# Kernel tuning notes

Hardware: AMD Instinct MI355X
Metric: run time of the kernel (lower is better)

The kernel has to match this reference:

```python
import jax, jax.numpy as jnp
import numpy as np

HEADS = 16
DIM_HEAD = 64
LN_EPS = 1e-3  # keras LayerNormalization default


def setup_inputs() -> dict:
    key = jax.random.key(0)
    ks = jax.random.split(key, 4)
    B, N, D = 8, 512, 1024
    inner = HEADS * DIM_HEAD  # 1024
    return {
        "x": jax.random.normal(ks[0], (B, N, D), dtype=jnp.float32),
        "w_qkv": jax.random.normal(ks[1], (D, 3 * inner), dtype=jnp.float32) * (D ** -0.5),
        "reattn_w": jax.random.normal(ks[2], (HEADS, HEADS), dtype=jnp.float32),
        "ln_gamma": jnp.ones((HEADS,), dtype=jnp.float32),
        "ln_beta": jnp.zeros((HEADS,), dtype=jnp.float32),
        "w_out": jax.random.normal(ks[3], (inner, D), dtype=jnp.float32) * (inner ** -0.5),
        "b_out": jnp.zeros((D,), dtype=jnp.float32),
    }


def reference(x, w_qkv, reattn_w, ln_gamma, ln_beta, w_out, b_out):
    B, N, D = x.shape
    H, dh = HEADS, DIM_HEAD
    scale = dh ** -0.5

    qkv = x @ w_qkv  # [B, N, 3*H*dh]
    q, k, v = jnp.split(qkv, 3, axis=-1)
    # b n (h d) -> b h n d
    to_heads = lambda t: t.reshape(B, N, H, dh).transpose(0, 2, 1, 3)
    q, k, v = to_heads(q), to_heads(k), to_heads(v)

    dots = jnp.einsum("bhid,bhjd->bhij", q, k) * scale  # [B, H, N, N]
    attn = jax.nn.softmax(dots, axis=-1)

    # re-attention: mix across heads
    attn = jnp.einsum("bhij,hg->bgij", attn, reattn_w)

    # LayerNorm over the head axis (axis=1), keras default eps
    mean = jnp.mean(attn, axis=1, keepdims=True)
    var = jnp.var(attn, axis=1, keepdims=True)
    attn = (attn - mean) * jax.lax.rsqrt(var + LN_EPS)
    attn = attn * ln_gamma[None, :, None, None] + ln_beta[None, :, None, None]

    out = jnp.einsum("bhij,bhjd->bhid", attn, v)  # [B, H, N, dh]
    out = out.transpose(0, 2, 1, 3).reshape(B, N, H * dh)  # b h n d -> b n (h d)
    return out @ w_out + b_out
```

## Files before the change

### kernel.cpp

```cpp
#include <hip/hip_runtime.h>
#include <math.h>

#define BB 8
#define NN 512
#define DD 1024
#define HH 16
#define DH 64
#define INNER 1024
#define QKV3 3072
#define PSTR (NN * NN + 64)

typedef __attribute__((ext_vector_type(8))) short short8;
typedef __attribute__((ext_vector_type(4))) float f32x4;

#define AS1 __attribute__((address_space(1)))
#define AS3 __attribute__((address_space(3)))

__device__ __forceinline__ float4 ld4(const float* p) { return *(const float4*)p; }

__device__ __forceinline__ unsigned short f2bf(float f) {
    unsigned u = __float_as_uint(f);
    return (unsigned short)((u + 0x7fffu + ((u >> 16) & 1u)) >> 16);
}
__device__ __forceinline__ float bf2f(unsigned short u) {
    return __uint_as_float(((unsigned)u) << 16);
}

__global__ void preprocess(const float* __restrict__ x, unsigned short* __restrict__ xb,
                           const float* __restrict__ wq, unsigned short* __restrict__ wqT,
                           const float* __restrict__ wo, unsigned short* __restrict__ woT) {
    __shared__ float t[32][33];
    const int tid = threadIdx.x;
    const int bx = blockIdx.x;
    if (bx < 4096) {
        size_t i = ((size_t)bx * 256 + tid) * 4;
        float4 v = ld4(x + i);
        ushort4 o;
        o.x = f2bf(v.x); o.y = f2bf(v.y); o.z = f2bf(v.z); o.w = f2bf(v.w);
        *(ushort4*)(xb + i) = o;
        return;
    }
    const float* in; unsigned short* out; int K, N, n0, k0;
    if (bx < 7168) {
        const int bb = bx - 4096;
        in = wq; out = wqT; K = DD; N = QKV3;
        n0 = (bb % 96) * 32; k0 = (bb / 96) * 32;
    } else {
        const int bb = bx - 7168;
        in = wo; out = woT; K = INNER; N = INNER;
        n0 = (bb & 31) * 32; k0 = (bb >> 5) * 32;
    }
    const int tx = tid & 31, ty = tid >> 5;
#pragma unroll
    for (int l = 0; l < 4; ++l)
        t[ty + 8 * l][tx] = in[(size_t)(k0 + ty + 8 * l) * N + n0 + tx];
    __syncthreads();
#pragma unroll
    for (int l = 0; l < 4; ++l)
        out[(size_t)(n0 + ty + 8 * l) * K + k0 + tx] = f2bf(t[tx][ty + 8 * l]);
}

__device__ __forceinline__ void stage128(const unsigned short* __restrict__ A,
                                         const unsigned short* __restrict__ Bt,
                                         int K, int bm, int bn, int kt,
                                         short* sb, int w, int l) {
#pragma unroll
    for (int t = 0; t < 2; ++t) {
        const int q = w * 2 + t;
        const int li = q * 512 + l * 8;
        const int row = li >> 5, kc = li & 31;
        __builtin_amdgcn_global_load_lds(
            (const AS1 void*)(A + (size_t)(bm + row) * K + kt * 32 + kc),
            (AS3 void*)(sb + q * 512), 16, 0, 0);
        __builtin_amdgcn_global_load_lds(
            (const AS1 void*)(Bt + (size_t)(bn + row) * K + kt * 32 + kc),
            (AS3 void*)(sb + 4096 + q * 512), 16, 0, 0);
    }
}

__global__ __launch_bounds__(256) void gemm_bf16(
    const unsigned short* __restrict__ A, const unsigned short* __restrict__ Bt,
    float* __restrict__ C, const float* __restrict__ bias, int M, int N, int K) {
    __shared__ __align__(16) short lds_[2 * 8192];
    const int tid = threadIdx.x;
    const int w = tid >> 6, l = tid & 63;
    const int bm = blockIdx.y * 128, bn = blockIdx.x * 128;
    const int wm = (w >> 1) * 64, wn = (w & 1) * 64;
    const int lrow = l & 15, lq = l >> 4;
    const int NT = K >> 5;

    f32x4 acc[4][4];
#pragma unroll
    for (int i = 0; i < 4; ++i)
#pragma unroll
        for (int j = 0; j < 4; ++j) acc[i][j] = (f32x4){0.f, 0.f, 0.f, 0.f};

    stage128(A, Bt, K, bm, bn, 0, lds_, w, l);
    asm volatile("s_waitcnt vmcnt(0)" ::: "memory");
    __builtin_amdgcn_s_barrier();

    for (int t = 0; t < NT; ++t) {
        const int s = t & 1;
        if (t + 1 < NT)
            stage128(A, Bt, K, bm, bn, t + 1, lds_ + (s ^ 1) * 8192, w, l);
        const short* As_ = lds_ + s * 8192;
        const short* Bs_ = As_ + 4096;
        short8 a[4], b[4];
#pragma unroll
        for (int i = 0; i < 4; ++i)
            a[i] = *(const short8*)(As_ + (wm + i * 16 + lrow) * 32 + lq * 8);
#pragma unroll
        for (int j = 0; j < 4; ++j)
            b[j] = *(const short8*)(Bs_ + (wn + j * 16 + lrow) * 32 + lq * 8);

        asm volatile("s_waitcnt lgkmcnt(0)" ::: "memory");
        __builtin_amdgcn_sched_barrier(0);

        __builtin_amdgcn_s_setprio(1);
#pragma unroll
        for (int i = 0; i < 4; ++i)
#pragma unroll
            for (int j = 0; j < 4; ++j)
                acc[i][j] = __builtin_amdgcn_mfma_f32_16x16x32_bf16(a[i], b[j], acc[i][j], 0, 0, 0);
        __builtin_amdgcn_s_setprio(0);

        asm volatile("s_waitcnt vmcnt(0)" ::: "memory");
        __builtin_amdgcn_s_barrier();
    }

#pragma unroll
    for (int i = 0; i < 4; ++i)
#pragma unroll
        for (int j = 0; j < 4; ++j) {
            const int col = bn + wn + j * 16 + lrow;
            const float bv = bias ? bias[col] : 0.f;
#pragma unroll
            for (int r = 0; r < 4; ++r) {
                const int row = bm + wm + i * 16 + lq * 4 + r;
                C[(size_t)row * N + col] = acc[i][j][r] + bv;
            }
        }
}

__device__ __forceinline__ void stage_st(const unsigned short* __restrict__ G, int K,
                                         int row0, int kt, short* dst_half,
                                         int w, int l) {
    const int grow = row0 + w * 16 + (l >> 2);
    const int gcol = kt * 32 + (((l & 3) * 8) ^ ((l & 32) ? 16 : 0));
    __builtin_amdgcn_global_load_lds(
        (const AS1 void*)(G + (size_t)grow * K + gcol),
        (AS3 void*)(dst_half + w * 512), 16, 0, 0);
}

__global__ __launch_bounds__(512, 2) void gemm256_bf(
    const unsigned short* __restrict__ A, const unsigned short* __restrict__ Bt,
    unsigned short* __restrict__ C, int M, int N, int K) {
    __shared__ __align__(16) short lds_[2 * 16384];
    const int tid = threadIdx.x;
    const int w = tid >> 6, l = tid & 63;
    const int wm = w >> 2, wn = w & 3;
    const int lrow = l & 15, lq = l >> 4;
    const int bm = blockIdx.y * 256, bn = blockIdx.x * 256;
    const int NT = K >> 5;

    const int aoff = lrow * 32 + ((lq * 8) ^ ((lrow & 8) ? 16 : 0));
    const int bsub = (wn & 1) * 4;

    f32x4 acc[8][4];
#pragma unroll
    for (int i = 0; i < 8; ++i)
#pragma unroll
        for (int j = 0; j < 4; ++j) acc[i][j] = (f32x4){0.f, 0.f, 0.f, 0.f};

    stage_st(A,  K, bm,       0, lds_ + 0,     w, l);
    stage_st(A,  K, bm + 128, 0, lds_ + 4096,  w, l);
    stage_st(Bt, K, bn,       0, lds_ + 8192,  w, l);
    stage_st(Bt, K, bn + 128, 0, lds_ + 12288, w, l);
    asm volatile("s_waitcnt vmcnt(0)" ::: "memory");
    __builtin_amdgcn_s_barrier();

    for (int t = 0; t < NT; ++t) {
        const int s = t & 1;
        if (t + 1 < NT) {
            short* nb = lds_ + (s ^ 1) * 16384;
            stage_st(A,  K, bm,       t + 1, nb,         w, l);
            stage_st(A,  K, bm + 128, t + 1, nb + 4096,  w, l);
            stage_st(Bt, K, bn,       t + 1, nb + 8192,  w, l);
            stage_st(Bt, K, bn + 128, t + 1, nb + 12288, w, l);
        }
        const short* Ah = lds_ + s * 16384 + wm * 4096;
        const short* Bh = lds_ + s * 16384 + 8192 + (wn >> 1) * 4096;
        short8 a[8], bfr[4];
#pragma unroll
        for (int i = 0; i < 8; ++i)
            a[i] = *(const short8*)(Ah + i * 512 + aoff);
#pragma unroll
        for (int j = 0; j < 4; ++j)
            bfr[j] = *(const short8*)(Bh + (bsub + j) * 512 + aoff);

        asm volatile("s_waitcnt lgkmcnt(0)" ::: "memory");
        __builtin_amdgcn_sched_barrier(0);

        __builtin_amdgcn_s_setprio(1);
#pragma unroll
        for (int i = 0; i < 8; ++i)
#pragma unroll
            for (int j = 0; j < 4; ++j)
                acc[i][j] = __builtin_amdgcn_mfma_f32_16x16x32_bf16(a[i], bfr[j], acc[i][j], 0, 0, 0);
        __builtin_amdgcn_s_setprio(0);

        asm volatile("s_waitcnt vmcnt(0)" ::: "memory");
        __builtin_amdgcn_s_barrier();
    }

#pragma unroll
    for (int fr = 0; fr < 8; ++fr)
#pragma unroll
        for (int fc = 0; fc < 4; ++fc) {
            const int col = bn + wn * 64 + fc * 16 + lrow;
#pragma unroll
            for (int r = 0; r < 4; ++r) {
                const int row = bm + wm * 128 + fr * 16 + lq * 4 + r;
                C[(size_t)row * N + col] = f2bf(acc[fr][fc][r]);
            }
        }
}

__global__ __launch_bounds__(256) void scores_stream(
    const unsigned short* __restrict__ qkvb, unsigned short* __restrict__ attnb,
    float* __restrict__ lsum2) {
    __shared__ unsigned short Ks[256 * 64];
    __shared__ unsigned short obuf[4][16][68];
    const int bh = blockIdx.x;
    const int h = bh & 15, b = bh >> 4;
    const int jh = blockIdx.y;
    const int w = threadIdx.x >> 6, l = threadIdx.x & 63;
    const int i0 = blockIdx.z * 64 + w * 16;
    const int lrow = l & 15, lq = l >> 4;

    const unsigned short* kbase =
        qkvb + (size_t)(b * NN + jh * 256) * QKV3 + INNER + h * DH;
#pragma unroll
    for (int i = 0; i < 8; ++i) {
        const int r = (w * 8 + i) * 8 + (l >> 3);
        const int c = (l & 7) ^ (r & 7);
        __builtin_amdgcn_global_load_lds(
            (const AS1 void*)(kbase + (size_t)r * QKV3 + c * 8),
            (AS3 void*)(Ks + (w * 8 + i) * 512), 16, 0, 0);
    }

    const unsigned short* qb = qkvb + (size_t)(b * NN) * QKV3 + h * DH + lq * 8;
    const short8 qf0 = *(const short8*)(qb + (size_t)(i0 + lrow) * QKV3);
    const short8 qf1 = *(const short8*)(qb + (size_t)(i0 + lrow) * QKV3 + 32);

    asm volatile("s_waitcnt vmcnt(0)" ::: "memory");
    __syncthreads();

    unsigned short* obase = attnb + (size_t)bh * PSTR + (size_t)i0 * NN + jh * 256;
    const int sw = lrow & 7;
    float lacc = 0.f;
#pragma unroll
    for (int jt = 0; jt < 16; ++jt) {
        const int R = jt * 16 + lrow;
        const short8 kf0 = *(const short8*)(Ks + R * 64 + ((lq ^ sw) * 8));
        const short8 kf1 = *(const short8*)(Ks + R * 64 + (((4 + lq) ^ sw) * 8));
        f32x4 acc = (f32x4){0.f, 0.f, 0.f, 0.f};
        acc = __builtin_amdgcn_mfma_f32_16x16x32_bf16(kf0, qf0, acc, 0, 0, 0);
        acc = __builtin_amdgcn_mfma_f32_16x16x32_bf16(kf1, qf1, acc, 0, 0, 0);
        float e0 = __expf(acc[0] * 0.125f);
        float e1 = __expf(acc[1] * 0.125f);
        float e2 = __expf(acc[2] * 0.125f);
        float e3 = __expf(acc[3] * 0.125f);
        lacc += (e0 + e1) + (e2 + e3);
        ushort4 o;
        o.x = f2bf(e0); o.y = f2bf(e1); o.z = f2bf(e2); o.w = f2bf(e3);
        *(ushort4*)(&obuf[w][lrow][(jt & 3) * 16 + lq * 4]) = o;
        if ((jt & 3) == 3) {
            const int jb = (jt >> 2) * 64;
#pragma unroll
            for (int q = 0; q < 4; ++q) {
                const int rr = q * 4 + (l >> 4);
                const int cc = l & 15;
                *(ushort4*)(obase + (size_t)rr * NN + jb + cc * 4) =
                    *(const ushort4*)(&obuf[w][rr][cc * 4]);
            }
        }
    }
    lacc += __shfl_xor(lacc, 16, 64);
    lacc += __shfl_xor(lacc, 32, 64);
    if (lq == 0)
        lsum2[(size_t)jh * BB * HH * NN + (size_t)bh * NN + i0 + lrow] = lacc;
}

__global__ void reattn_ln_bf(unsigned short* __restrict__ attnb,
                             const float* __restrict__ lsum2,
                             const float* __restrict__ rw,
                             const float* __restrict__ gamma,
                             const float* __restrict__ beta) {
    __shared__ float w[16][16];
    __shared__ float gs[16], bs[16];
    const int tid = threadIdx.x;
    ((float*)w)[tid] = rw[tid];
    if (tid < 16) { gs[tid] = gamma[tid]; bs[tid] = beta[tid]; }
    __syncthreads();

    const size_t idx = (size_t)blockIdx.x * 256 + tid;
    const int j4 = (int)(idx & 127);
    const int i = (int)((idx >> 7) & 511);
    const int b = (int)(idx >> 16);
    unsigned short* base = attnb + (size_t)(b * HH) * PSTR + (size_t)i * NN + j4 * 4;
    const float* l0 = lsum2 + (size_t)(b * HH) * NN + i;
    const float* l1 = l0 + (size_t)BB * HH * NN;

    float v[16][4];
#pragma unroll
    for (int h = 0; h < 16; ++h) {
        const float linv = 1.0f / (l0[h * NN] + l1[h * NN]);
        ushort4 u = *(const ushort4*)(base + (size_t)h * PSTR);
        v[h][0] = bf2f(u.x) * linv; v[h][1] = bf2f(u.y) * linv;
        v[h][2] = bf2f(u.z) * linv; v[h][3] = bf2f(u.w) * linv;
    }
    float o[16][4];
    float me[4] = {0.f, 0.f, 0.f, 0.f};
#pragma unroll
    for (int g = 0; g < 16; ++g) {
        float s0 = 0.f, s1 = 0.f, s2 = 0.f, s3 = 0.f;
#pragma unroll
        for (int h = 0; h < 16; ++h) {
            const float wg = w[h][g];
            s0 += v[h][0] * wg; s1 += v[h][1] * wg;
            s2 += v[h][2] * wg; s3 += v[h][3] * wg;
        }
        o[g][0] = s0; o[g][1] = s1; o[g][2] = s2; o[g][3] = s3;
        me[0] += s0; me[1] += s1; me[2] += s2; me[3] += s3;
    }
#pragma unroll
    for (int r = 0; r < 4; ++r) me[r] *= 0.0625f;
    float va[4] = {0.f, 0.f, 0.f, 0.f};
#pragma unroll
    for (int g = 0; g < 16; ++g)
#pragma unroll
        for (int r = 0; r < 4; ++r) {
            float d = o[g][r] - me[r];
            va[r] += d * d;
        }
    float ri[4];
#pragma unroll
    for (int r = 0; r < 4; ++r) ri[r] = rsqrtf(va[r] * 0.0625f + 1e-3f);
#pragma unroll
    for (int g = 0; g < 16; ++g) {
        ushort4 u;
        u.x = f2bf((o[g][0] - me[0]) * ri[0] * gs[g] + bs[g]);
        u.y = f2bf((o[g][1] - me[1]) * ri[1] * gs[g] + bs[g]);
        u.z = f2bf((o[g][2] - me[2]) * ri[2] * gs[g] + bs[g]);
        u.w = f2bf((o[g][3] - me[3]) * ri[3] * gs[g] + bs[g]);
        *(ushort4*)(base + (size_t)g * PSTR) = u;
    }
}

__global__ void transpose_v(const unsigned short* __restrict__ qkvb,
                            unsigned short* __restrict__ vT) {
    __shared__ unsigned short t[32][33];
    const int bh = blockIdx.z;
    const int h = bh & 15, b = bh >> 4;
    const int j0 = blockIdx.x * 32, d0 = blockIdx.y * 32;
    const int tx = threadIdx.x & 31, ty = threadIdx.x >> 5;
    const unsigned short* src = qkvb + (size_t)(b * NN) * QKV3 + 2 * INNER + h * DH;
#pragma unroll
    for (int k = 0; k < 4; ++k)
        t[ty + 8 * k][tx] = src[(size_t)(j0 + ty + 8 * k) * QKV3 + d0 + tx];
    __syncthreads();
    unsigned short* dst = vT + (size_t)bh * DH * NN;
#pragma unroll
    for (int k = 0; k < 4; ++k)
        dst[(size_t)(d0 + ty + 8 * k) * NN + j0 + tx] = t[tx][ty + 8 * k];
}

__device__ __forceinline__ void stage_pv(const unsigned short* __restrict__ pb,
                                         const unsigned short* __restrict__ vb,
                                         int j0, short* Ps, short* Vs,
                                         int w, int l, int lr8, int swd) {
#pragma unroll
    for (int t = 0; t < 4; ++t) {
        int c = w * 4 + t;
        int r = c * 8 + lr8;
        __builtin_amdgcn_global_load_lds(
            (const AS1 void*)(pb + (size_t)r * NN + j0 + swd),
            (AS3 void*)(Ps + c * 512), 16, 0, 0);
    }
#pragma unroll
    for (int t = 0; t < 2; ++t) {
        int c = w * 2 + t;
        int d = c * 8 + lr8;
        __builtin_amdgcn_global_load_lds(
            (const AS1 void*)(vb + (size_t)d * NN + j0 + swd),
            (AS3 void*)(Vs + c * 512), 16, 0, 0);
    }
}

__global__ __launch_bounds__(256) void pv_mfma(
    const unsigned short* __restrict__ attnb, const unsigned short* __restrict__ vT,
    unsigned short* __restrict__ outhb) {
    const int bh = blockIdx.x;
    const int h = bh & 15, b = bh >> 4;
    const int i0 = blockIdx.y * 128;
    __shared__ __align__(16) short Ps[2][128 * 64];
    __shared__ __align__(16) short Vs[2][64 * 64];
    const int tid = threadIdx.x;
    const int w = tid >> 6, l = tid & 63;
    const int lrow = l & 15, lq = l >> 4;
    const int lr8 = l >> 3;
    const int swd = ((l & 7) ^ (lr8 & 7)) * 8;

    f32x4 acc[2][4];
#pragma unroll
    for (int ic = 0; ic < 2; ++ic)
#pragma unroll
        for (int dt = 0; dt < 4; ++dt) acc[ic][dt] = (f32x4){0.f, 0.f, 0.f, 0.f};

    const unsigned short* pb = attnb + (size_t)bh * PSTR + (size_t)i0 * NN;
    const unsigned short* vb = vT + (size_t)bh * DH * NN;

    stage_pv(pb, vb, 0, Ps[0], Vs[0], w, l, lr8, swd);
    asm volatile("s_waitcnt vmcnt(0)" ::: "memory");
    __builtin_amdgcn_s_barrier();

    for (int js = 0; js < 8; ++js) {
        const int s = js & 1;
        if (js + 1 < 8)
            stage_pv(pb, vb, (js + 1) * 64, Ps[s ^ 1], Vs[s ^ 1], w, l, lr8, swd);

        short8 vf[8], pf[4];
#pragma unroll
        for (int kh = 0; kh < 2; ++kh) {
#pragma unroll
            for (int dt = 0; dt < 4; ++dt)
                vf[kh * 4 + dt] = *(const short8*)(
                    &Vs[s][(dt * 16 + lrow) * 64 + (((kh * 4 + lq) ^ (lrow & 7)) * 8)]);
#pragma unroll
            for (int ic = 0; ic < 2; ++ic)
                pf[kh * 2 + ic] = *(const short8*)(
                    &Ps[s][(w * 32 + ic * 16 + lrow) * 64 + (((kh * 4 + lq) ^ (lrow & 7)) * 8)]);
        }

        asm volatile("s_waitcnt lgkmcnt(0)" ::: "memory");
        __builtin_amdgcn_sched_barrier(0);

        __builtin_amdgcn_s_setprio(1);
#pragma unroll
        for (int kh = 0; kh < 2; ++kh)
#pragma unroll
            for (int ic = 0; ic < 2; ++ic)
#pragma unroll
                for (int dt = 0; dt < 4; ++dt)
                    acc[ic][dt] = __builtin_amdgcn_mfma_f32_16x16x32_bf16(
                        vf[kh * 4 + dt], pf[kh * 2 + ic], acc[ic][dt], 0, 0, 0);
        __builtin_amdgcn_s_setprio(0);

        asm volatile("s_waitcnt vmcnt(0)" ::: "memory");
        __builtin_amdgcn_s_barrier();
    }

#pragma unroll
    for (int ic = 0; ic < 2; ++ic) {
        unsigned short* orow = outhb +
            ((size_t)(b * NN + i0 + w * 32 + ic * 16 + lrow)) * INNER + h * DH + lq * 4;
#pragma unroll
        for (int dt = 0; dt < 4; ++dt) {
            ushort4 o;
            o.x = f2bf(acc[ic][dt][0]); o.y = f2bf(acc[ic][dt][1]);
            o.z = f2bf(acc[ic][dt][2]); o.w = f2bf(acc[ic][dt][3]);
            *(ushort4*)(orow + dt * 16) = o;
        }
    }
}

extern "C" void kernel_launch(void* const* d_in, const int* in_sizes, int n_in,
                              void* d_out, int out_size, void* d_ws, size_t ws_size,
                              hipStream_t stream) {
    const float* x        = (const float*)d_in[0];
    const float* w_qkv    = (const float*)d_in[1];
    const float* reattn_w = (const float*)d_in[2];
    const float* ln_gamma = (const float*)d_in[3];
    const float* ln_beta  = (const float*)d_in[4];
    const float* w_out    = (const float*)d_in[5];
    const float* b_out    = (const float*)d_in[6];
    float* out = (float*)d_out;

    unsigned short* qkvb  = (unsigned short*)d_ws;
    unsigned short* attnb = qkvb + (size_t)BB * NN * QKV3;
    unsigned short* vTb   = attnb + (size_t)BB * HH * PSTR;
    unsigned short* outhb = vTb + (size_t)BB * HH * DH * NN;
    unsigned short* xb    = outhb + (size_t)BB * NN * INNER;
    unsigned short* wqkvT = xb + (size_t)BB * NN * DD;
    unsigned short* woutT = wqkvT + (size_t)DD * QKV3;
    float*          lsum2 = (float*)(woutT + (size_t)INNER * INNER);

    dim3 blk(256);

    preprocess<<<dim3(8192), blk, 0, stream>>>(x, xb, w_qkv, wqkvT, w_out, woutT);

    gemm256_bf<<<dim3(QKV3 / 256, (BB * NN) / 256), dim3(512), 0, stream>>>(
        xb, wqkvT, qkvb, BB * NN, QKV3, DD);

    scores_stream<<<dim3(BB * HH, 2, NN / 64), blk, 0, stream>>>(qkvb, attnb, lsum2);

    reattn_ln_bf<<<dim3((BB * NN * NN) / 1024), blk, 0, stream>>>(
        attnb, lsum2, reattn_w, ln_gamma, ln_beta);

    transpose_v<<<dim3(NN / 32, DH / 32, BB * HH), blk, 0, stream>>>(qkvb, vTb);

    pv_mfma<<<dim3(BB * HH, NN / 128), blk, 0, stream>>>(attnb, vTb, outhb);

    gemm_bf16<<<dim3(INNER / 128, (BB * NN) / 128), blk, 0, stream>>>(
        outhb, woutT, out, b_out, BB * NN, INNER, INNER);
}
```

Baseline: 208.4 us.

## Shrink QKV GEMM tile to 256x128 and merge V transpose into scores kernel

New measurement: 201.9 us (median of 2 runs). 1.03x faster.

```diff
diff --git a/kernel.cpp b/kernel.cpp
--- a/kernel.cpp
+++ b/kernel.cpp
@@ -152,61 +152,57 @@
         (AS3 void*)(dst_half + w * 512), 16, 0, 0);
 }
 
-__global__ __launch_bounds__(512, 2) void gemm256_bf(
+__global__ __launch_bounds__(512, 4) void gemm256_bf(
     const unsigned short* __restrict__ A, const unsigned short* __restrict__ Bt,
     unsigned short* __restrict__ C, int M, int N, int K) {
-    __shared__ __align__(16) short lds_[2 * 16384];
+    __shared__ __align__(16) short lds_[2 * 12288];
     const int tid = threadIdx.x;
     const int w = tid >> 6, l = tid & 63;
-    const int wm = w >> 2, wn = w & 3;
+    const int wmi = w >> 1, wni = w & 1;
     const int lrow = l & 15, lq = l >> 4;
-    const int bm = blockIdx.y * 256, bn = blockIdx.x * 256;
+    const int bm = blockIdx.y * 256, bn = blockIdx.x * 128;
     const int NT = K >> 5;
 
     const int aoff = lrow * 32 + ((lq * 8) ^ ((lrow & 8) ? 16 : 0));
-    const int bsub = (wn & 1) * 4;
-
-    f32x4 acc[8][4];
-#pragma unroll
-    for (int i = 0; i < 8; ++i)
+
+    f32x4 acc[4][4];
+#pragma unroll
+    for (int i = 0; i < 4; ++i)
 #pragma unroll
         for (int j = 0; j < 4; ++j) acc[i][j] = (f32x4){0.f, 0.f, 0.f, 0.f};
 
-    stage_st(A,  K, bm,       0, lds_ + 0,     w, l);
-    stage_st(A,  K, bm + 128, 0, lds_ + 4096,  w, l);
-    stage_st(Bt, K, bn,       0, lds_ + 8192,  w, l);
-    stage_st(Bt, K, bn + 128, 0, lds_ + 12288, w, l);
+    stage_st(A,  K, bm,       0, lds_ + 0,    w, l);
+    stage_st(A,  K, bm + 128, 0, lds_ + 4096, w, l);
+    stage_st(Bt, K, bn,       0, lds_ + 8192, w, l);
     asm volatile("s_waitcnt vmcnt(0)" ::: "memory");
     __builtin_amdgcn_s_barrier();
 
     for (int t = 0; t < NT; ++t) {
         const int s = t & 1;
         if (t + 1 < NT) {
-            short* nb = lds_ + (s ^ 1) * 16384;
-            stage_st(A,  K, bm,       t + 1, nb,         w, l);
-            stage_st(A,  K, bm + 128, t + 1, nb + 4096,  w, l);
-            stage_st(Bt, K, bn,       t + 1, nb + 8192,  w, l);
-            stage_st(Bt, K, bn + 128, t + 1, nb + 12288, w, l);
-        }
-        const short* Ah = lds_ + s * 16384 + wm * 4096;
-        const short* Bh = lds_ + s * 16384 + 8192 + (wn >> 1) * 4096;
-        short8 a[8], bfr[4];
-#pragma unroll
-        for (int i = 0; i < 8; ++i)
-            a[i] = *(const short8*)(Ah + i * 512 + aoff);
+            short* nb = lds_ + (s ^ 1) * 12288;
+            stage_st(A,  K, bm,       t + 1, nb,        w, l);
+            stage_st(A,  K, bm + 128, t + 1, nb + 4096, w, l);
+            stage_st(Bt, K, bn,       t + 1, nb + 8192, w, l);
+        }
+        const short* cb = lds_ + s * 12288;
+        short8 a[4], b[4];
+#pragma unroll
+        for (int i = 0; i < 4; ++i)
+            a[i] = *(const short8*)(cb + (wmi * 4 + i) * 512 + aoff);
 #pragma unroll
         for (int j = 0; j < 4; ++j)
-            bfr[j] = *(const short8*)(Bh + (bsub + j) * 512 + aoff);
+            b[j] = *(const short8*)(cb + 8192 + (wni * 4 + j) * 512 + aoff);
 
         asm volatile("s_waitcnt lgkmcnt(0)" ::: "memory");
         __builtin_amdgcn_sched_barrier(0);
 
         __builtin_amdgcn_s_setprio(1);
 #pragma unroll
-        for (int i = 0; i < 8; ++i)
+        for (int i = 0; i < 4; ++i)
 #pragma unroll
             for (int j = 0; j < 4; ++j)
-                acc[i][j] = __builtin_amdgcn_mfma_f32_16x16x32_bf16(a[i], bfr[j], acc[i][j], 0, 0, 0);
+                acc[i][j] = __builtin_amdgcn_mfma_f32_16x16x32_bf16(a[i], b[j], acc[i][j], 0, 0, 0);
         __builtin_amdgcn_s_setprio(0);
 
         asm volatile("s_waitcnt vmcnt(0)" ::: "memory");
@@ -214,28 +210,52 @@
     }
 
 #pragma unroll
-    for (int fr = 0; fr < 8; ++fr)
-#pragma unroll
-        for (int fc = 0; fc < 4; ++fc) {
-            const int col = bn + wn * 64 + fc * 16 + lrow;
+    for (int i = 0; i < 4; ++i)
+#pragma unroll
+        for (int j = 0; j < 4; ++j) {
+            const int col = bn + wni * 64 + j * 16 + lrow;
 #pragma unroll
             for (int r = 0; r < 4; ++r) {
-                const int row = bm + wm * 128 + fr * 16 + lq * 4 + r;
-                C[(size_t)row * N + col] = f2bf(acc[fr][fc][r]);
+                const int row = bm + wmi * 64 + i * 16 + lq * 4 + r;
+                C[(size_t)row * N + col] = f2bf(acc[i][j][r]);
             }
         }
 }
 
-__global__ __launch_bounds__(256) void scores_stream(
+__global__ __launch_bounds__(256) void scores_tv(
     const unsigned short* __restrict__ qkvb, unsigned short* __restrict__ attnb,
-    float* __restrict__ lsum2) {
-    __shared__ unsigned short Ks[256 * 64];
-    __shared__ unsigned short obuf[4][16][68];
-    const int bh = blockIdx.x;
+    unsigned short* __restrict__ vT, float* __restrict__ lsum2) {
+    __shared__ unsigned short sh[256 * 64 + 4 * 16 * 68];
+    const int bx = blockIdx.x;
+    const int tid = threadIdx.x;
+
+    if (bx >= 2048) {
+        const int t = bx - 2048;
+        const int j0 = (t & 15) * 32;
+        const int d0 = ((t >> 4) & 1) * 32;
+        const int bh = t >> 5;
+        const int h = bh & 15, b = bh >> 4;
+        unsigned short (*tt)[33] = (unsigned short(*)[33])sh;
+        const int tx = tid & 31, ty = tid >> 5;
+        const unsigned short* src = qkvb + (size_t)(b * NN) * QKV3 + 2 * INNER + h * DH;
+#pragma unroll
+        for (int k = 0; k < 4; ++k)
+            tt[ty + 8 * k][tx] = src[(size_t)(j0 + ty + 8 * k) * QKV3 + d0 + tx];
+        __syncthreads();
+        unsigned short* dst = vT + (size_t)bh * DH * NN;
+#pragma unroll
+        for (int k = 0; k < 4; ++k)
+            dst[(size_t)(d0 + ty + 8 * k) * NN + j0 + tx] = tt[tx][ty + 8 * k];
+        return;
+    }
+
+    unsigned short* Ks = sh;
+    unsigned short* obuf = sh + 16384;
+    const int bh = bx & 127;
     const int h = bh & 15, b = bh >> 4;
-    const int jh = blockIdx.y;
-    const int w = threadIdx.x >> 6, l = threadIdx.x & 63;
-    const int i0 = blockIdx.z * 64 + w * 16;
+    const int jh = (bx >> 7) & 1;
+    const int w = tid >> 6, l = tid & 63;
+    const int i0 = (bx >> 8) * 64 + w * 16;
     const int lrow = l & 15, lq = l >> 4;
 
     const unsigned short* kbase =
@@ -257,6 +277,7 @@
     __syncthreads();
 
     unsigned short* obase = attnb + (size_t)bh * PSTR + (size_t)i0 * NN + jh * 256;
+    unsigned short* ob = obuf + (w * 16) * 68;
     const int sw = lrow & 7;
     float lacc = 0.f;
 #pragma unroll
@@ -274,7 +295,7 @@
         lacc += (e0 + e1) + (e2 + e3);
         ushort4 o;
         o.x = f2bf(e0); o.y = f2bf(e1); o.z = f2bf(e2); o.w = f2bf(e3);
-        *(ushort4*)(&obuf[w][lrow][(jt & 3) * 16 + lq * 4]) = o;
+        *(ushort4*)(ob + lrow * 68 + (jt & 3) * 16 + lq * 4) = o;
         if ((jt & 3) == 3) {
             const int jb = (jt >> 2) * 64;
 #pragma unroll
@@ -282,7 +303,7 @@
                 const int rr = q * 4 + (l >> 4);
                 const int cc = l & 15;
                 *(ushort4*)(obase + (size_t)rr * NN + jb + cc * 4) =
-                    *(const ushort4*)(&obuf[w][rr][cc * 4]);
+                    *(const ushort4*)(ob + rr * 68 + cc * 4);
             }
         }
     }
@@ -356,24 +377,6 @@
         u.w = f2bf((o[g][3] - me[3]) * ri[3] * gs[g] + bs[g]);
         *(ushort4*)(base + (size_t)g * PSTR) = u;
     }
-}
-
-__global__ void transpose_v(const unsigned short* __restrict__ qkvb,
-                            unsigned short* __restrict__ vT) {
-    __shared__ unsigned short t[32][33];
-    const int bh = blockIdx.z;
-    const int h = bh & 15, b = bh >> 4;
-    const int j0 = blockIdx.x * 32, d0 = blockIdx.y * 32;
-    const int tx = threadIdx.x & 31, ty = threadIdx.x >> 5;
-    const unsigned short* src = qkvb + (size_t)(b * NN) * QKV3 + 2 * INNER + h * DH;
-#pragma unroll
-    for (int k = 0; k < 4; ++k)
-        t[ty + 8 * k][tx] = src[(size_t)(j0 + ty + 8 * k) * QKV3 + d0 + tx];
-    __syncthreads();
-    unsigned short* dst = vT + (size_t)bh * DH * NN;
-#pragma unroll
-    for (int k = 0; k < 4; ++k)
-        dst[(size_t)(d0 + ty + 8 * k) * NN + j0 + tx] = t[tx][ty + 8 * k];
 }
 
 __device__ __forceinline__ void stage_pv(const unsigned short* __restrict__ pb,
@@ -500,16 +503,14 @@
 
     preprocess<<<dim3(8192), blk, 0, stream>>>(x, xb, w_qkv, wqkvT, w_out, woutT);
 
-    gemm256_bf<<<dim3(QKV3 / 256, (BB * NN) / 256), dim3(512), 0, stream>>>(
+    gemm256_bf<<<dim3(QKV3 / 128, (BB * NN) / 256), dim3(512), 0, stream>>>(
         xb, wqkvT, qkvb, BB * NN, QKV3, DD);
 
-    scores_stream<<<dim3(BB * HH, 2, NN / 64), blk, 0, stream>>>(qkvb, attnb, lsum2);
+    scores_tv<<<dim3(6144), blk, 0, stream>>>(qkvb, attnb, vTb, lsum2);
 
     reattn_ln_bf<<<dim3((BB * NN * NN) / 1024), blk, 0, stream>>>(
         attnb, lsum2, reattn_w, ln_gamma, ln_beta);
 
-    transpose_v<<<dim3(NN / 32, DH / 32, BB * HH), blk, 0, stream>>>(qkvb, vTb);
-
     pv_mfma<<<dim3(BB * HH, NN / 128), blk, 0, stream>>>(attnb, vTb, outhb);
 
     gemm_bf16<<<dim3(INNER / 128, (BB * NN) / 128), blk, 0, stream>>>(
```
